# Kernel optimization log

Measured on AMD Instinct MI355X. Metric: run time of the kernel, lower is better.

## Reference

```python
import jax, jax.numpy as jnp
import numpy as np

B, T, I, H, O = 64, 256, 128, 512, 64
GRAD_CLIP = 5.0


def setup_inputs() -> dict:
    key = jax.random.key(0)
    ks = jax.random.split(key, 20)
    sH = 1.0 / np.sqrt(H)
    sI = 1.0 / np.sqrt(I)
    f32 = jnp.float32
    return {
        "x": jax.random.normal(ks[0], (B, T, I), f32),
        "y": jax.random.randint(ks[1], (B,), 0, O),
        "W1w": jax.random.normal(ks[2], (H, H), f32) * sH,
        "V1w": jax.random.normal(ks[3], (H, I), f32) * sI,
        "V1b": jnp.zeros((H,), f32),
        "W2w": jax.random.normal(ks[4], (H, H), f32) * sH,
        "W2b": jnp.zeros((H,), f32),
        "V2w": jax.random.normal(ks[5], (H, I), f32) * sI,
        "W3w": jax.random.normal(ks[6], (H, H), f32) * sH,
        "W3b": jnp.zeros((H,), f32),
        "V3w": jax.random.normal(ks[7], (H, I), f32) * sI,
        "Woutw": jax.random.normal(ks[8], (O, H), f32) * sH,
        "Woutb": jnp.zeros((O,), f32),
        "BW1": jax.random.normal(ks[9], (O, H), f32) * sH,
        "BV1": jax.random.normal(ks[10], (O, H), f32) * sH,
        "BW2": jax.random.normal(ks[11], (O, H), f32) * sH,
        "BV2": jax.random.normal(ks[12], (O, H), f32) * sH,
        "BW3": jax.random.normal(ks[13], (O, H), f32) * sH,
        "BV3": jax.random.normal(ks[14], (O, H), f32) * sH,
    }


def reference(x, y, W1w, V1w, V1b, W2w, W2b, V2w, W3w, W3b, V3w,
              Woutw, Woutb, BW1, BV1, BW2, BV2, BW3, BV3):
    Bsz, Tlen, _ = x.shape
    Hd = W1w.shape[0]
    Od = Woutw.shape[0]
    h0 = jnp.zeros((Bsz, Hd), x.dtype)
    xt = jnp.swapaxes(x, 0, 1)  # [T, B, I]

    def step(h, xti):
        z = jax.nn.sigmoid(h @ W2w.T + W2b + xti @ V2w.T)
        r = jax.nn.sigmoid(h @ W3w.T + W3b + xti @ V3w.T)
        ht = jnp.tanh(xti @ V1w.T + V1b + (h * r) @ W1w.T)
        hn = (1.0 - z) * ht + z * h
        return hn, (r, z, ht, hn)

    hT, (rs, zs, hs, hid) = jax.lax.scan(step, h0, xt)  # each [T, B, H]
    output = jax.nn.softmax(hT @ Woutw.T + Woutb, axis=-1)
    error = output - jax.nn.one_hot(y, Od, dtype=output.dtype)

    BW1e, BV1e = error @ BW1, error @ BV1
    BW2e, BV2e = error @ BW2, error @ BV2
    BW3e, BV3e = error @ BW3, error @ BV3

    hiddens = jnp.concatenate([h0[None], hid], axis=0)  # [T+1, B, H]
    # Faithfully replicate torch's hiddens[t-1] list indexing: at t=0 this is
    # hiddens[-1], i.e. the FINAL hidden state (Python negative indexing).
    idx = (np.arange(Tlen) - 1) % (Tlen + 1)
    hprev = hiddens[idx]  # [T, B, H]

    rr = rs * (1.0 - rs)
    sz = 1.0 - zs
    dh = 1.0 - hs ** 2

    # z-gate terms (index 1) -- original code uses r*(1-r) here, replicated.
    zg = (hprev - hs) * rr
    zgV = zg * BV2e[None]
    zgW = zg * BW2e[None]
    dV1 = jnp.einsum('tbh,tbi->hi', zgV, xt) / Bsz
    dW1 = jnp.einsum('tbh,tbH->hH', zgW, hprev) / Bsz
    db1 = zgV.sum(0).mean(0)

    # r-gate terms (index 2)
    AV = ((BV3e[None] * sz * dh) @ W1w.T) * hprev * rr
    AW = ((BW3e[None] * sz * dh) @ W1w.T) * hprev * rr
    dV2 = jnp.einsum('tbh,tbi->hi', AV, xt) / Bsz
    dW2 = jnp.einsum('tbh,tbH->hH', AW, hprev) / Bsz
    db2 = AV.sum(0).mean(0)

    # h-gate terms (index 0)
    HV = ((BV1e[None] * sz) @ W1w.T) * dh
    HW = ((BW1e[None] * sz) @ W1w.T) * dh
    dV0 = jnp.einsum('tbh,tbi->hi', HV, xt) / Bsz
    dW0 = jnp.einsum('tbh,tbH->hH', HW, rs * hprev) / Bsz
    db0 = HV.sum(0).mean(0)

    def nc(g):
        g = g / jnp.linalg.norm(g)
        return jnp.clip(g, -GRAD_CLIP, GRAD_CLIP)

    return (output, hT,
            nc(dW0), nc(dW1), nc(dW2),
            nc(dV0), nc(dV1), nc(dV2),
            nc(db0), nc(db1), nc(db2),
            error)
```

## Files before the change

### kernel.cpp

```cpp
#include <hip/hip_runtime.h>
#include <hip/hip_bf16.h>

#define DI __device__ __forceinline__

typedef __bf16 bf16x8 __attribute__((ext_vector_type(8)));
typedef __bf16 bf16x4 __attribute__((ext_vector_type(4)));
typedef __bf16 bf16x2 __attribute__((ext_vector_type(2)));
typedef float  f32x4  __attribute__((ext_vector_type(4)));
typedef unsigned long long ull;

static constexpr int Bc = 64, Tc = 256, Ic = 128, Hc = 512, Oc = 64;
static constexpr int TBc = Tc * Bc;
static constexpr size_t THW = (size_t)TBc * Hc;

static constexpr size_t O_OUT = 0;
static constexpr size_t O_HT  = 4096;
static constexpr size_t O_DW0 = 36864;
static constexpr size_t O_DV0 = 823296;
static constexpr size_t O_DB0 = 1019904;
static constexpr size_t O_ERR = 1021440;

static constexpr size_t W_SLOT = 1024;
static constexpr size_t W_DB   = 2048;
static constexpr size_t W_FLG  = 8192;
static constexpr size_t W_ERRW = 16384;
static constexpr size_t W_PROJ = 32768;
static constexpr size_t W_W1B  = 819200;
static constexpr size_t W_HX   = 1343488;
static constexpr size_t W_HRX  = 1474560;
static constexpr size_t W_XT   = 1605632;
static constexpr size_t W_HIST = 5799936;
static constexpr size_t W_PB   = 72908800;
static constexpr size_t W_NEED = W_PB + 100663296;


DI void st32_agent(float* p, float v) {
  __hip_atomic_store((unsigned int*)p, __float_as_uint(v),
                     __ATOMIC_RELAXED, __HIP_MEMORY_SCOPE_AGENT);
}
DI ull ld64_agent(const void* p) {
  return __hip_atomic_load((ull*)p, __ATOMIC_RELAXED, __HIP_MEMORY_SCOPE_AGENT);
}

DI void group_barrier(int* flags_g, int myslot, int bar, bool& dead) {
  __syncthreads();
  if (threadIdx.x == 0)
    __hip_atomic_store(&flags_g[myslot * 32], bar,
                       __ATOMIC_RELAXED, __HIP_MEMORY_SCOPE_AGENT);
  if (threadIdx.x < 64 && !dead) {
    const int l = threadIdx.x;
    int spins = 0;
    for (;;) {
      int v = bar;
      if (l < 16)
        v = __hip_atomic_load(&flags_g[l * 32],
                              __ATOMIC_RELAXED, __HIP_MEMORY_SCOPE_AGENT);
      if (__all(v >= bar)) break;
      __builtin_amdgcn_s_sleep(1);
      if (++spins > 4000000) { dead = true; break; }
    }
  }
  __syncthreads();
}

DI float hprev_at(const __bf16* __restrict__ h_h, int k, int col) {
  int t = k >> 6;
  if (t == 1) return 0.f;
  int row = (t == 0) ? (16320 + (k & 63)) : (k - 128);
  return (float)h_h[(size_t)row * 512 + col];
}


__global__ void kzero(float* __restrict__ p, int n) {
  int i = blockIdx.x * 256 + threadIdx.x;
  if (i < n) p[i] = 0.f;
}
__global__ void ksent(float* p, float v) { p[0] = v; }

__global__ __launch_bounds__(256)
void k1_xv(const float* __restrict__ x, const float* __restrict__ V1w,
           const float* __restrict__ V2w, const float* __restrict__ V3w,
           const float* __restrict__ V1b, const float* __restrict__ W2b,
           const float* __restrict__ W3b,
           float* __restrict__ xv1f, float* __restrict__ xv2f, float* __restrict__ xv3f)
{
  const int cb = blockIdx.x, t = blockIdx.y;
  const int g = cb >> 3, jblk = cb & 7;
  const float* Vg   = (g == 0) ? V1w : (g == 1) ? V2w : V3w;
  const float* bias = (g == 0) ? V1b : (g == 1) ? W2b : W3b;
  float* of = (g == 0) ? xv1f : (g == 1) ? xv2f : xv3f;
  __shared__ float As[64 * 69];
  __shared__ float Bs[64 * 69];
  const int tid = threadIdx.x;
  float acc[4][4] = {};
  const int m0 = (tid & 15) * 4, j0 = (tid >> 4) * 4;
  for (int kc = 0; kc < 2; ++kc) {
    __syncthreads();
    #pragma unroll
    for (int e = 0; e < 4; ++e) {
      int idx = tid + e * 256;
      int row = idx >> 4, c4 = (idx & 15) * 4;
      float4 v = *reinterpret_cast<const float4*>(&x[((size_t)row * 256 + t) * 128 + kc * 64 + c4]);
      As[row * 69 + c4 + 0] = v.x; As[row * 69 + c4 + 1] = v.y;
      As[row * 69 + c4 + 2] = v.z; As[row * 69 + c4 + 3] = v.w;
      float4 w = *reinterpret_cast<const float4*>(&Vg[(size_t)(jblk * 64 + row) * 128 + kc * 64 + c4]);
      Bs[row * 69 + c4 + 0] = w.x; Bs[row * 69 + c4 + 1] = w.y;
      Bs[row * 69 + c4 + 2] = w.z; Bs[row * 69 + c4 + 3] = w.w;
    }
    __syncthreads();
    for (int i = 0; i < 64; ++i) {
      float a[4], b[4];
      #pragma unroll
      for (int u = 0; u < 4; ++u) a[u] = As[(m0 + u) * 69 + i];
      #pragma unroll
      for (int u = 0; u < 4; ++u) b[u] = Bs[(j0 + u) * 69 + i];
      #pragma unroll
      for (int mi = 0; mi < 4; ++mi)
        #pragma unroll
        for (int ji = 0; ji < 4; ++ji) acc[mi][ji] += a[mi] * b[ji];
    }
  }
  #pragma unroll
  for (int ji = 0; ji < 4; ++ji) {
    int jg = jblk * 64 + j0 + ji;
    float bv = bias[jg];
    #pragma unroll
    for (int mi = 0; mi < 4; ++mi) {
      int b = m0 + mi;
      of[((size_t)t * 64 + b) * 512 + jg] = acc[mi][ji] + bv;
    }
  }
}

__global__ __launch_bounds__(256, 1)
void k2_recur(const float* __restrict__ W1w, const float* __restrict__ W2w,
              const float* __restrict__ W3w,
              const float* __restrict__ xv1, const float* __restrict__ xv2,
              const float* __restrict__ xv3,
              __bf16* __restrict__ r_h, __bf16* __restrict__ z_h,
              __bf16* __restrict__ ht_h, __bf16* __restrict__ h_h,
              float* __restrict__ hx, float* __restrict__ hrx,
              int* __restrict__ flags, float* __restrict__ dout,
              const float* __restrict__ x, __bf16* __restrict__ XT,
              __bf16* __restrict__ W1b)
{
  __shared__ __align__(16) char smem[37376];
  const int tid = threadIdx.x;
  const int bid = blockIdx.x;

  if (bid >= 64) {
    if (bid < 320) {
      const int t = bid - 64;
      __bf16* xs = (__bf16*)smem;
      #pragma unroll
      for (int e = 0; e < 8; ++e) {
        int idx = tid + e * 256;
        int b = idx >> 5, c4 = (idx & 31) * 4;
        float4 v = *reinterpret_cast<const float4*>(&x[((size_t)b * 256 + t) * 128 + c4]);
        xs[b * 132 + c4 + 0] = (__bf16)v.x; xs[b * 132 + c4 + 1] = (__bf16)v.y;
        xs[b * 132 + c4 + 2] = (__bf16)v.z; xs[b * 132 + c4 + 3] = (__bf16)v.w;
      }
      __syncthreads();
      #pragma unroll
      for (int e = 0; e < 8; ++e) {
        int idx = tid + e * 256;
        int i = idx >> 4, b4 = (idx & 15) * 4;
        __bf16* d = &XT[(size_t)i * TBc + t * 64 + b4];
        d[0] = xs[(b4 + 0) * 132 + i];
        d[1] = xs[(b4 + 1) * 132 + i];
        d[2] = xs[(b4 + 2) * 132 + i];
        d[3] = xs[(b4 + 3) * 132 + i];
      }
    } else if (bid < 352) {
      for (int i = (bid - 320) * 256 + tid; i < 262144; i += 32 * 256)
        W1b[i] = (__bf16)W1w[i];
    } else {
      float* p = dout + O_DW0;
      for (int i = (bid - 352) * 256 + tid; i < 983040; i += 64 * 256)
        p[i] = 0.f;
    }
    return;
  }

  const int g  = bid >> 4;
  const int cw = bid & 15;
  const int lane = tid & 63, wv = tid >> 6;
  const int kh = wv & 1;
  const int ct = wv >> 1;
  const int q  = lane >> 4;
  const int colc = cw * 32 + ct * 16 + (lane & 15);
  const bool owner = (kh == 0);

  __bf16* c0  = (__bf16*)smem;
  __bf16* c1  = (__bf16*)(smem + 16384);
  float*  pbuf = (float*)(smem + 32768);

  bf16x8 w1c[2][8], w2c[2][8], w3c[2][8];
  #pragma unroll
  for (int kk2 = 0; kk2 < 8; ++kk2) {
    const int kb = (kh * 8 + kk2) * 32 + q * 8;
    #pragma unroll
    for (int j = 0; j < 8; ++j) {
      float w = W1w[(size_t)colc * 512 + kb + j];
      __bf16 a = (__bf16)w;
      w1c[0][kk2][j] = a; w1c[1][kk2][j] = (__bf16)(w - (float)a);
      w = W2w[(size_t)colc * 512 + kb + j];
      a = (__bf16)w;
      w2c[0][kk2][j] = a; w2c[1][kk2][j] = (__bf16)(w - (float)a);
      w = W3w[(size_t)colc * 512 + kb + j];
      a = (__bf16)w;
      w3c[0][kk2][j] = a; w3c[1][kk2][j] = (__bf16)(w - (float)a);
    }
  }
  for (int i = tid; i < 8192; i += 256) {
    c0[i] = (__bf16)0.f; c1[i] = (__bf16)0.f;
  }
  __syncthreads();

  float hreg[4] = {0.f, 0.f, 0.f, 0.f};
  float* hx_g  = hx  + g * 8192;
  float* hrx_g = hrx + g * 8192;
  int* flags_g = flags + g * 16 * 32;
  const int fragbase = (colc >> 5) * 512 + (((colc >> 3) & 3) * 16 + q * 4) * 8 + (colc & 7);
  const int pb = (ct * 64 + lane) * 9;

  auto stage = [&](const float* __restrict__ srcf) {
    const ull* src = reinterpret_cast<const ull*>(srcf);
    ull u[16];
    #pragma unroll
    for (int j = 0; j < 16; ++j) u[j] = ld64_agent(src + j * 256 + tid);
    #pragma unroll
    for (int j = 0; j < 16; ++j) {
      float f0 = __uint_as_float((unsigned int)u[j]);
      float f1 = __uint_as_float((unsigned int)(u[j] >> 32));
      __bf16 a0 = (__bf16)f0; __bf16 b0 = (__bf16)(f0 - (float)a0);
      __bf16 a1 = (__bf16)f1; __bf16 b1 = (__bf16)(f1 - (float)a1);
      int o = (j * 256 + tid) * 2;
      bf16x2 v0; v0[0] = a0; v0[1] = a1;
      bf16x2 v1; v1[0] = b0; v1[1] = b1;
      *reinterpret_cast<bf16x2*>(&c0[o]) = v0;
      *reinterpret_cast<bf16x2*>(&c1[o]) = v1;
    }
  };

  bool dead = false;
  int bar = 0;
  #pragma unroll 1
  for (int t = 0; t < Tc; ++t) {
    const size_t rowb = ((size_t)t * 64 + g * 16 + q * 4) * 512 + colc;
    float xv1v[4], xv2v[4], xv3v[4];
    if (owner) {
      #pragma unroll
      for (int i = 0; i < 4; ++i) {
        size_t o = rowb + (size_t)i * 512;
        xv1v[i] = xv1[o]; xv2v[i] = xv2[o]; xv3v[i] = xv3[o];
      }
    }
    f32x4 a2 = {0.f,0.f,0.f,0.f}, a3 = {0.f,0.f,0.f,0.f};
    #pragma unroll
    for (int kk2 = 0; kk2 < 8; ++kk2) {
      const int idx = (kh * 8 + kk2) * 512 + lane * 8;
      bf16x8 h0 = *reinterpret_cast<const bf16x8*>(&c0[idx]);
      bf16x8 h1 = *reinterpret_cast<const bf16x8*>(&c1[idx]);
      a2 = __builtin_amdgcn_mfma_f32_16x16x32_bf16(h0, w2c[0][kk2], a2, 0, 0, 0);
      a2 = __builtin_amdgcn_mfma_f32_16x16x32_bf16(h1, w2c[0][kk2], a2, 0, 0, 0);
      a2 = __builtin_amdgcn_mfma_f32_16x16x32_bf16(h0, w2c[1][kk2], a2, 0, 0, 0);
      a3 = __builtin_amdgcn_mfma_f32_16x16x32_bf16(h0, w3c[0][kk2], a3, 0, 0, 0);
      a3 = __builtin_amdgcn_mfma_f32_16x16x32_bf16(h1, w3c[0][kk2], a3, 0, 0, 0);
      a3 = __builtin_amdgcn_mfma_f32_16x16x32_bf16(h0, w3c[1][kk2], a3, 0, 0, 0);
    }
    if (!owner) {
      #pragma unroll
      for (int i = 0; i < 4; ++i) { pbuf[pb + i] = a2[i]; pbuf[pb + 4 + i] = a3[i]; }
    }
    __syncthreads();
    float zz[4], rr4[4];
    if (owner) {
      #pragma unroll
      for (int i = 0; i < 4; ++i) {
        float s2 = a2[i] + pbuf[pb + i]     + xv2v[i];
        float s3 = a3[i] + pbuf[pb + 4 + i] + xv3v[i];
        zz[i]  = 1.f / (1.f + expf(-s2));
        rr4[i] = 1.f / (1.f + expf(-s3));
        st32_agent(&hrx_g[fragbase + i * 8], hreg[i] * rr4[i]);
      }
    }
    ++bar; group_barrier(flags_g, cw, bar, dead);
    if (owner) {
      #pragma unroll
      for (int i = 0; i < 4; ++i) {
        z_h[rowb + (size_t)i * 512] = (__bf16)zz[i];
        r_h[rowb + (size_t)i * 512] = (__bf16)rr4[i];
      }
    }
    stage(hrx_g);
    __syncthreads();
    f32x4 a1 = {0.f,0.f,0.f,0.f};
    #pragma unroll
    for (int kk2 = 0; kk2 < 8; ++kk2) {
      const int idx = (kh * 8 + kk2) * 512 + lane * 8;
      bf16x8 h0 = *reinterpret_cast<const bf16x8*>(&c0[idx]);
      bf16x8 h1 = *reinterpret_cast<const bf16x8*>(&c1[idx]);
      a1 = __builtin_amdgcn_mfma_f32_16x16x32_bf16(h0, w1c[0][kk2], a1, 0, 0, 0);
      a1 = __builtin_amdgcn_mfma_f32_16x16x32_bf16(h1, w1c[0][kk2], a1, 0, 0, 0);
      a1 = __builtin_amdgcn_mfma_f32_16x16x32_bf16(h0, w1c[1][kk2], a1, 0, 0, 0);
    }
    if (!owner) {
      #pragma unroll
      for (int i = 0; i < 4; ++i) pbuf[pb + i] = a1[i];
    }
    __syncthreads();
    float htv[4];
    if (owner) {
      #pragma unroll
      for (int i = 0; i < 4; ++i) {
        float pre = a1[i] + pbuf[pb + i] + xv1v[i];
        float ht = tanhf(pre);
        float hn = zz[i] * (hreg[i] - ht) + ht;
        htv[i] = ht;
        hreg[i] = hn;
        st32_agent(&hx_g[fragbase + i * 8], hn);
      }
    }
    ++bar; group_barrier(flags_g, cw, bar, dead);
    if (owner) {
      #pragma unroll
      for (int i = 0; i < 4; ++i) {
        ht_h[rowb + (size_t)i * 512] = (__bf16)htv[i];
        h_h[rowb + (size_t)i * 512]  = (__bf16)hreg[i];
      }
    }
    if (t + 1 < Tc) stage(hx_g);
    __syncthreads();
  }
  if (owner) {
    #pragma unroll
    for (int i = 0; i < 4; ++i) {
      int b = g * 16 + q * 4 + i;
      dout[O_HT + (size_t)b * 512 + colc] = hreg[i];
    }
  }
}

__global__ void k3a_soft(const float* __restrict__ Woutw, const float* __restrict__ Woutb,
                         const int* __restrict__ y, float* __restrict__ dout,
                         float* __restrict__ errw)
{
  const int b = blockIdx.x, o = threadIdx.x;
  const float* hrow = dout + O_HT + (size_t)b * 512;
  float sv = Woutb[o];
  for (int k = 0; k < 512; ++k) sv += hrow[k] * Woutw[(size_t)o * 512 + k];
  float mx = sv;
  for (int off = 32; off; off >>= 1) mx = fmaxf(mx, __shfl_xor(mx, off, 64));
  float e = expf(sv - mx);
  float sum = e;
  for (int off = 32; off; off >>= 1) sum += __shfl_xor(sum, off, 64);
  float outp = e / sum;
  float errv = outp - ((y[b] == o) ? 1.f : 0.f);
  dout[O_OUT + b * 64 + o] = outp;
  dout[O_ERR + b * 64 + o] = errv;
  errw[b * 64 + o] = errv;
}

__global__ __launch_bounds__(256)
void k3b_proj(const float* __restrict__ err,
              const float* b0, const float* b1, const float* b2,
              const float* b3, const float* b4, const float* b5,
              float* __restrict__ proj)
{
  const int p = blockIdx.y;
  const int hb = blockIdx.x * 64;
  const float* BX = (p==0)?b0:(p==1)?b1:(p==2)?b2:(p==3)?b3:(p==4)?b4:b5;
  __shared__ float es[64 * 64];
  __shared__ float bs[64 * 65];
  for (int i = threadIdx.x; i < 4096; i += 256) es[i] = err[i];
  for (int i = threadIdx.x; i < 4096; i += 256) {
    int o = i >> 6, hh = i & 63;
    bs[o * 65 + hh] = BX[(size_t)o * 512 + hb + hh];
  }
  __syncthreads();
  for (int e = 0; e < 16; ++e) {
    int idx = threadIdx.x + e * 256;
    int b = idx >> 6, hh = idx & 63;
    float s = 0.f;
    for (int o = 0; o < 64; ++o) s += es[b * 64 + o] * bs[o * 65 + hh];
    proj[(size_t)p * 32768 + b * 512 + hb + hh] = s;
  }
}

__global__ __launch_bounds__(256)
void e1t(const __bf16* __restrict__ r_h, const __bf16* __restrict__ h_h,
         __bf16* __restrict__ HpT, __bf16* __restrict__ RsHpT)
{
  const int t = blockIdx.y, hb = blockIdx.x * 64;
  const int tid = threadIdx.x;
  __shared__ __bf16 tr[64 * 68];
  float hpv[16], rv[16];
  #pragma unroll
  for (int e = 0; e < 16; ++e) {
    int idx = tid + e * 256;
    int b = idx >> 6, hl = idx & 63;
    hpv[e] = hprev_at(h_h, t * 64 + b, hb + hl);
    rv[e]  = (float)r_h[((size_t)t * 64 + b) * 512 + hb + hl];
  }
  for (int rnd = 0; rnd < 2; ++rnd) {
    __syncthreads();
    #pragma unroll
    for (int e = 0; e < 16; ++e) {
      int idx = tid + e * 256;
      int b = idx >> 6, hl = idx & 63;
      tr[b * 68 + hl] = (__bf16)(rnd == 0 ? hpv[e] : rv[e] * hpv[e]);
    }
    __syncthreads();
    __bf16* dst = (rnd == 0) ? HpT : RsHpT;
    #pragma unroll
    for (int e = 0; e < 16; ++e) {
      int idx = tid + e * 256;
      int hl2 = idx >> 6, b2 = idx & 63;
      dst[(size_t)(hb + hl2) * TBc + t * 64 + b2] = tr[b2 * 68 + hl2];
    }
  }
}

__global__ __launch_bounds__(256)
void k4_pgemm(const __bf16* __restrict__ z_h, const __bf16* __restrict__ ht_h,
              const __bf16* __restrict__ r_h, const __bf16* __restrict__ h_h,
              const float* __restrict__ proj, const __bf16* __restrict__ W1b,
              __bf16* __restrict__ P)
{
  const int p = blockIdx.z;
  const int krow0 = blockIdx.x * 128;
  const int n0 = blockIdx.y * 128;
  const int pidx = (p == 0) ? 5 : (p == 1) ? 4 : (p == 2) ? 1 : 0;
  const float* pr = proj + (size_t)pidx * 32768;
  const int tid = threadIdx.x, lane = tid & 63, wv = tid >> 6, q = lane >> 4;
  const int wm = (wv & 1) * 64, wn = (wv >> 1) * 64;
  __shared__ __align__(16) __bf16 Al[128 * 40];
  __shared__ __align__(16) __bf16 Bl[128 * 40];
  f32x4 acc[4][4] = {};
  for (int kt = 0; kt < 16; ++kt) {
    const int h0 = kt * 32;
    __syncthreads();
    #pragma unroll
    for (int e = 0; e < 4; ++e) {
      int idx = tid + e * 256;
      int row = idx >> 3, h4 = (idx & 7) * 4;
      int kg = krow0 + row;
      bf16x4 zz = *reinterpret_cast<const bf16x4*>(&z_h[(size_t)kg * 512 + h0 + h4]);
      bf16x4 tt = *reinterpret_cast<const bf16x4*>(&ht_h[(size_t)kg * 512 + h0 + h4]);
      float4 pv = *reinterpret_cast<const float4*>(&pr[(size_t)(kg & 63) * 512 + h0 + h4]);
      float pvv[4] = {pv.x, pv.y, pv.z, pv.w};
      bf16x4 gv;
      #pragma unroll
      for (int j = 0; j < 4; ++j) {
        float sz = 1.f - (float)zz[j];
        float v = pvv[j] * sz;
        if (p < 2) { float h = (float)tt[j]; v *= (1.f - h * h); }
        gv[j] = (__bf16)v;
      }
      *reinterpret_cast<bf16x4*>(&Al[row * 40 + h4]) = gv;
      bf16x4 wv4 = *reinterpret_cast<const bf16x4*>(&W1b[(size_t)(n0 + row) * 512 + h0 + h4]);
      *reinterpret_cast<bf16x4*>(&Bl[row * 40 + h4]) = wv4;
    }
    __syncthreads();
    bf16x8 af[4], bfv[4];
    #pragma unroll
    for (int mi = 0; mi < 4; ++mi)
      af[mi] = *reinterpret_cast<const bf16x8*>(&Al[(wm + mi * 16 + (lane & 15)) * 40 + q * 8]);
    #pragma unroll
    for (int ni = 0; ni < 4; ++ni)
      bfv[ni] = *reinterpret_cast<const bf16x8*>(&Bl[(wn + ni * 16 + (lane & 15)) * 40 + q * 8]);
    #pragma unroll
    for (int mi = 0; mi < 4; ++mi)
      #pragma unroll
      for (int ni = 0; ni < 4; ++ni)
        acc[mi][ni] = __builtin_amdgcn_mfma_f32_16x16x32_bf16(af[mi], bfv[ni], acc[mi][ni], 0, 0, 0);
  }
  __bf16* Pp = P + (size_t)p * THW;
  #pragma unroll
  for (int mi = 0; mi < 4; ++mi) {
    const int kg = krow0 + wm + mi * 16 + q * 4;
    const int tt = kg >> 6;
    #pragma unroll
    for (int ni = 0; ni < 4; ++ni) {
      const int n = n0 + wn + ni * 16 + (lane & 15);
      union { __bf16 b[4]; uint2 u; } pk;
      #pragma unroll
      for (int i = 0; i < 4; ++i) {
        float mul;
        if (p < 2) {
          float r = (float)r_h[(size_t)(kg + i) * 512 + n];
          float hp = 0.f;
          if (tt != 1) {
            int kr = (tt == 0) ? (16320 + (kg & 63) + i) : (kg + i - 128);
            hp = (float)h_h[(size_t)kr * 512 + n];
          }
          mul = hp * r * (1.f - r);
        } else {
          float h = (float)ht_h[(size_t)(kg + i) * 512 + n];
          mul = 1.f - h * h;
        }
        pk.b[i] = (__bf16)(acc[mi][ni][i] * mul);
      }
      *reinterpret_cast<uint2*>(&Pp[(size_t)n * TBc + kg]) = pk.u;
    }
  }
}

__global__ __launch_bounds__(256)
void k5_all(const __bf16* __restrict__ P, const __bf16* __restrict__ RsHpT,
            const __bf16* __restrict__ HpT, const __bf16* __restrict__ XT,
            const __bf16* __restrict__ r_h, const __bf16* __restrict__ ht_h,
            const __bf16* __restrict__ h_h, const float* __restrict__ proj,
            float* __restrict__ dout, float scale)
{
  const __bf16* Ap; int amode; const __bf16* Bp; const float* projA;
  float* out; int N; int m0i, n0i, zi;
  int b = blockIdx.x;
  if (b < 768) {
    int job = b >> 8, wb = b & 255;
    m0i = wb & 3; n0i = (wb >> 2) & 3; zi = wb >> 4;
    N = 512;
    out = dout + O_DW0 + (size_t)job * 262144;
    if (job == 0)      { Ap = P + 3 * THW; amode = 0; Bp = RsHpT; projA = proj; }
    else if (job == 1) { Ap = nullptr;     amode = 1; Bp = HpT;   projA = proj + 2 * 32768; }
    else               { Ap = P + 1 * THW; amode = 0; Bp = HpT;   projA = proj; }
  } else {
    int b2 = b - 768; int job = b2 >> 6, wb = b2 & 63;
    m0i = wb & 3; n0i = 0; zi = wb >> 2;
    N = 128;
    out = dout + O_DV0 + (size_t)job * 65536;
    if (job == 0)      { Ap = P + 2 * THW; amode = 0; Bp = XT; projA = proj; }
    else if (job == 1) { Ap = nullptr;     amode = 1; Bp = XT; projA = proj + 3 * 32768; }
    else               { Ap = P + 0 * THW; amode = 0; Bp = XT; projA = proj; }
  }
  const int m0 = m0i * 128;
  const int n0 = n0i * 128;
  const int klen = 1024;
  const int tid = threadIdx.x, lane = tid & 63, wv = tid >> 6, q = lane >> 4;
  const int wm = (wv & 1) * 64, wn = (wv >> 1) * 64;
  __shared__ __align__(16) __bf16 Al[128 * 72];
  __shared__ __align__(16) __bf16 Bl[128 * 72];
  f32x4 acc[4][4] = {};
  const int iters = klen >> 6;
  for (int kt = 0; kt < iters; ++kt) {
    const int kk0 = zi * klen + kt * 64;
    __syncthreads();
    #pragma unroll
    for (int e = 0; e < 8; ++e) {
      int idx = tid + e * 256;
      int row = idx >> 4, c4 = (idx & 15) * 4;
      bf16x4 bv = *reinterpret_cast<const bf16x4*>(&Bp[(size_t)(n0 + row) * TBc + kk0 + c4]);
      *reinterpret_cast<bf16x4*>(&Bl[row * 72 + c4]) = bv;
    }
    if (amode == 0) {
      #pragma unroll
      for (int e = 0; e < 8; ++e) {
        int idx = tid + e * 256;
        int row = idx >> 4, c4 = (idx & 15) * 4;
        bf16x4 av = *reinterpret_cast<const bf16x4*>(&Ap[(size_t)(m0 + row) * TBc + kk0 + c4]);
        *reinterpret_cast<bf16x4*>(&Al[row * 72 + c4]) = av;
      }
    } else {
      #pragma unroll
      for (int e = 0; e < 8; ++e) {
        int idx = tid + e * 256;
        int kk = idx >> 5;
        int m4 = (idx & 31) * 4;
        int kg = kk0 + kk;
        int tt = kg >> 6;
        bf16x4 hs = *reinterpret_cast<const bf16x4*>(&ht_h[(size_t)kg * 512 + m0 + m4]);
        bf16x4 rv = *reinterpret_cast<const bf16x4*>(&r_h[(size_t)kg * 512 + m0 + m4]);
        float4 pv = *reinterpret_cast<const float4*>(&projA[(size_t)(kg & 63) * 512 + m0 + m4]);
        float pvv[4] = {pv.x, pv.y, pv.z, pv.w};
        float hpf[4] = {0.f, 0.f, 0.f, 0.f};
        if (tt != 1) {
          int kr = (tt == 0) ? (16320 + (kg & 63)) : (kg - 128);
          bf16x4 hp = *reinterpret_cast<const bf16x4*>(&h_h[(size_t)kr * 512 + m0 + m4]);
          #pragma unroll
          for (int j = 0; j < 4; ++j) hpf[j] = (float)hp[j];
        }
        #pragma unroll
        for (int j = 0; j < 4; ++j) {
          float r = (float)rv[j];
          float zg = (hpf[j] - (float)hs[j]) * r * (1.f - r) * pvv[j];
          Al[(m4 + j) * 72 + kk] = (__bf16)zg;
        }
      }
    }
    __syncthreads();
    #pragma unroll
    for (int ks = 0; ks < 2; ++ks) {
      bf16x8 af[4], bfv[4];
      #pragma unroll
      for (int mi = 0; mi < 4; ++mi)
        af[mi] = *reinterpret_cast<const bf16x8*>(&Al[(wm + mi * 16 + (lane & 15)) * 72 + ks * 32 + q * 8]);
      #pragma unroll
      for (int ni = 0; ni < 4; ++ni)
        bfv[ni] = *reinterpret_cast<const bf16x8*>(&Bl[(wn + ni * 16 + (lane & 15)) * 72 + ks * 32 + q * 8]);
      #pragma unroll
      for (int mi = 0; mi < 4; ++mi)
        #pragma unroll
        for (int ni = 0; ni < 4; ++ni)
          acc[mi][ni] = __builtin_amdgcn_mfma_f32_16x16x32_bf16(af[mi], bfv[ni], acc[mi][ni], 0, 0, 0);
    }
  }
  #pragma unroll
  for (int mi = 0; mi < 4; ++mi) {
    const int m = m0 + wm + mi * 16 + q * 4;
    #pragma unroll
    for (int ni = 0; ni < 4; ++ni) {
      const int n = n0 + wn + ni * 16 + (lane & 15);
      #pragma unroll
      for (int i = 0; i < 4; ++i)
        atomicAdd(&out[(size_t)(m + i) * N + n], acc[mi][ni][i] * scale);
    }
  }
}

__global__ void k_dbP(const __bf16* __restrict__ P, float* __restrict__ db)
{
  const size_t plane = (blockIdx.y == 0) ? 2 : 0;
  const int dbo = (blockIdx.y == 0) ? 0 : 1024;
  const __bf16* row = P + plane * THW + (size_t)blockIdx.x * TBc;
  float sv = 0.f;
  for (int i = threadIdx.x; i < TBc; i += 256) sv += (float)row[i];
  for (int off = 32; off; off >>= 1) sv += __shfl_xor(sv, off, 64);
  __shared__ float red[4];
  if ((threadIdx.x & 63) == 0) red[threadIdx.x >> 6] = sv;
  __syncthreads();
  if (threadIdx.x == 0)
    atomicAdd(&db[dbo + blockIdx.x], (red[0] + red[1] + red[2] + red[3]) * (1.f / 64.f));
}

__global__ void k_dbzg(const __bf16* __restrict__ r_h, const __bf16* __restrict__ ht_h,
                       const __bf16* __restrict__ h_h, const float* __restrict__ proj,
                       float* __restrict__ db)
{
  const int hb = blockIdx.x * 64;
  const int col = hb + (threadIdx.x & 63);
  const int part = threadIdx.x >> 6;
  const int kb = blockIdx.y * 1024;
  float sum = 0.f;
  for (int k = kb + part; k < kb + 1024; k += 4) {
    float hs = (float)ht_h[(size_t)k * 512 + col];
    float r  = (float)r_h[(size_t)k * 512 + col];
    float hp = hprev_at(h_h, k, col);
    float pv = proj[3 * 32768 + (size_t)(k & 63) * 512 + col];
    sum += (hp - hs) * r * (1.f - r) * pv;
  }
  __shared__ float sred[4][64];
  sred[part][threadIdx.x & 63] = sum;
  __syncthreads();
  if (threadIdx.x < 64)
    atomicAdd(&db[512 + hb + threadIdx.x],
              (sred[0][threadIdx.x] + sred[1][threadIdx.x] +
               sred[2][threadIdx.x] + sred[3][threadIdx.x]) * (1.f / 64.f));
}

__global__ void k6a_sumsq(const float* __restrict__ dout, const float* __restrict__ db,
                          float* __restrict__ slots)
{
  const int yy = blockIdx.y;
  const float* src; int count;
  if (yy < 3)      { src = dout + O_DW0 + (size_t)yy * 262144; count = 262144; }
  else if (yy < 6) { src = dout + O_DV0 + (size_t)(yy - 3) * 65536; count = 65536; }
  else             { src = db + (size_t)(yy - 6) * 512; count = 512; }
  int start = blockIdx.x * 4096;
  if (start >= count) return;
  int end = min(start + 4096, count);
  float sp = 0.f;
  for (int i = start + threadIdx.x; i < end; i += 256) { float v = src[i]; sp += v * v; }
  for (int off = 32; off; off >>= 1) sp += __shfl_xor(sp, off, 64);
  __shared__ float red[4];
  if ((threadIdx.x & 63) == 0) red[threadIdx.x >> 6] = sp;
  __syncthreads();
  if (threadIdx.x == 0) atomicAdd(&slots[yy], red[0] + red[1] + red[2] + red[3]);
}

__global__ void k6b_write(const float* __restrict__ db,
                          const float* __restrict__ slots, float* __restrict__ dout)
{
  const int yy = blockIdx.y;
  const float* src; int count; size_t oo;
  if (yy < 3)      { oo = O_DW0 + (size_t)yy * 262144; src = dout + oo; count = 262144; }
  else if (yy < 6) { oo = O_DV0 + (size_t)(yy - 3) * 65536; src = dout + oo; count = 65536; }
  else             { oo = O_DB0 + (size_t)(yy - 6) * 512; src = db + (size_t)(yy - 6) * 512; count = 512; }
  int start = blockIdx.x * 4096;
  if (start >= count) return;
  int end = min(start + 4096, count);
  float inv = 1.f / sqrtf(slots[yy]);
  for (int i = start + threadIdx.x; i < end; i += 256) {
    float v = src[i] * inv;
    dout[oo + i] = fminf(fmaxf(v, -5.f), 5.f);
  }
}

extern "C" void kernel_launch(void* const* d_in, const int* in_sizes, int n_in,
                              void* d_out, int out_size, void* d_ws, size_t ws_size,
                              hipStream_t stream)
{
  const float* x     = (const float*)d_in[0];
  const int*   y     = (const int*)d_in[1];
  const float* W1w   = (const float*)d_in[2];
  const float* V1w   = (const float*)d_in[3];
  const float* V1b   = (const float*)d_in[4];
  const float* W2w   = (const float*)d_in[5];
  const float* W2b   = (const float*)d_in[6];
  const float* V2w   = (const float*)d_in[7];
  const float* W3w   = (const float*)d_in[8];
  const float* W3b   = (const float*)d_in[9];
  const float* V3w   = (const float*)d_in[10];
  const float* Woutw = (const float*)d_in[11];
  const float* Woutb = (const float*)d_in[12];
  const float* BW1   = (const float*)d_in[13];
  const float* BV1   = (const float*)d_in[14];
  const float* BW2   = (const float*)d_in[15];
  const float* BV2   = (const float*)d_in[16];
  const float* BW3   = (const float*)d_in[17];
  const float* BV3   = (const float*)d_in[18];
  float* dout = (float*)d_out;
  char* ws = (char*)d_ws;

  if (ws_size < W_NEED) { ksent<<<1, 1, 0, stream>>>(dout, (float)ws_size); return; }

  float*  slots = (float*)(ws + W_SLOT);
  float*  dbr   = (float*)(ws + W_DB);
  int*    flg   = (int*)(ws + W_FLG);
  float*  errw  = (float*)(ws + W_ERRW);
  float*  proj  = (float*)(ws + W_PROJ);
  __bf16* W1b   = (__bf16*)(ws + W_W1B);
  float*  hx    = (float*)(ws + W_HX);
  float*  hrx   = (float*)(ws + W_HRX);
  __bf16* XT    = (__bf16*)(ws + W_XT);
  __bf16* r_h   = (__bf16*)(ws + W_HIST);
  __bf16* z_h   = (__bf16*)(ws + W_HIST + 16777216);
  __bf16* ht_h  = (__bf16*)(ws + W_HIST + 33554432);
  __bf16* h_h   = (__bf16*)(ws + W_HIST + 50331648);
  char*   PB    = ws + W_PB;

  float* xv1 = (float*)PB;
  float* xv2 = (float*)(PB + 33554432);
  float* xv3 = (float*)(PB + 67108864);
  __bf16* P     = (__bf16*)PB;
  __bf16* HpT   = (__bf16*)(PB + 67108864);
  __bf16* RsHpT = (__bf16*)(PB + 83886080);

  kzero<<<16, 256, 0, stream>>>((float*)ws, 4096);
  k1_xv<<<dim3(24, 256), 256, 0, stream>>>(x, V1w, V2w, V3w, V1b, W2b, W3b, xv1, xv2, xv3);
  k2_recur<<<416, 256, 0, stream>>>(W1w, W2w, W3w, xv1, xv2, xv3,
                                    r_h, z_h, ht_h, h_h, hx, hrx, flg, dout,
                                    x, XT, W1b);
  k3a_soft<<<64, 64, 0, stream>>>(Woutw, Woutb, y, dout, errw);
  k3b_proj<<<dim3(8, 6), 256, 0, stream>>>(errw, BW1, BV1, BW2, BV2, BW3, BV3, proj);
  e1t<<<dim3(8, 256), 256, 0, stream>>>(r_h, h_h, HpT, RsHpT);
  k_dbzg<<<dim3(8, 16), 256, 0, stream>>>(r_h, ht_h, h_h, proj, dbr);

  k4_pgemm<<<dim3(128, 4, 4), 256, 0, stream>>>(z_h, ht_h, r_h, h_h, proj, W1b, P);
  const float sc = 1.f / 64.f;
  k5_all<<<960, 256, 0, stream>>>(P, RsHpT, HpT, XT, r_h, ht_h, h_h, proj, dout, sc);
  k_dbP<<<dim3(512, 2), 256, 0, stream>>>(P, dbr);
  k6a_sumsq<<<dim3(64, 9), 256, 0, stream>>>(dout, dbr, slots);
  k6b_write<<<dim3(64, 9), 256, 0, stream>>>(dbr, slots, dout);
}
```

Measured before the change: 2.372 ms.

## Merge backward kernels, share W1 tiles in pgemm, and use split-bf16 MFMA for input projection

Four changes at once. The input projection now runs on MFMA with a three-term bf16 hi/lo split that approximates fp32, and each block loops over all eight column blocks. The transpose kernel is folded into the softmax launch, and the two bias-reduction kernels are folded into the weight-gradient GEMM launch, cutting launch count. The P GEMM computes two projection planes per block so W1 tiles are loaded once for both. This trades extra registers and LDS for fewer launches and less reloading, with a small precision change in the input projection.

```diff
diff --git a/kernel.cpp b/kernel.cpp
--- a/kernel.cpp
+++ b/kernel.cpp
@@ -84,51 +84,67 @@
            const float* __restrict__ W3b,
            float* __restrict__ xv1f, float* __restrict__ xv2f, float* __restrict__ xv3f)
 {
-  const int cb = blockIdx.x, t = blockIdx.y;
-  const int g = cb >> 3, jblk = cb & 7;
+  const int t = blockIdx.x, g = blockIdx.y;
   const float* Vg   = (g == 0) ? V1w : (g == 1) ? V2w : V3w;
   const float* bias = (g == 0) ? V1b : (g == 1) ? W2b : W3b;
   float* of = (g == 0) ? xv1f : (g == 1) ? xv2f : xv3f;
-  __shared__ float As[64 * 69];
-  __shared__ float Bs[64 * 69];
-  const int tid = threadIdx.x;
-  float acc[4][4] = {};
-  const int m0 = (tid & 15) * 4, j0 = (tid >> 4) * 4;
-  for (int kc = 0; kc < 2; ++kc) {
-    __syncthreads();
-    #pragma unroll
-    for (int e = 0; e < 4; ++e) {
-      int idx = tid + e * 256;
-      int row = idx >> 4, c4 = (idx & 15) * 4;
-      float4 v = *reinterpret_cast<const float4*>(&x[((size_t)row * 256 + t) * 128 + kc * 64 + c4]);
-      As[row * 69 + c4 + 0] = v.x; As[row * 69 + c4 + 1] = v.y;
-      As[row * 69 + c4 + 2] = v.z; As[row * 69 + c4 + 3] = v.w;
-      float4 w = *reinterpret_cast<const float4*>(&Vg[(size_t)(jblk * 64 + row) * 128 + kc * 64 + c4]);
-      Bs[row * 69 + c4 + 0] = w.x; Bs[row * 69 + c4 + 1] = w.y;
-      Bs[row * 69 + c4 + 2] = w.z; Bs[row * 69 + c4 + 3] = w.w;
-    }
-    __syncthreads();
-    for (int i = 0; i < 64; ++i) {
-      float a[4], b[4];
-      #pragma unroll
-      for (int u = 0; u < 4; ++u) a[u] = As[(m0 + u) * 69 + i];
-      #pragma unroll
-      for (int u = 0; u < 4; ++u) b[u] = Bs[(j0 + u) * 69 + i];
-      #pragma unroll
-      for (int mi = 0; mi < 4; ++mi)
+  __shared__ __align__(16) __bf16 xs0[64 * 36];
+  __shared__ __align__(16) __bf16 xs1[64 * 36];
+  __shared__ __align__(16) __bf16 vs0[64 * 36];
+  __shared__ __align__(16) __bf16 vs1[64 * 36];
+  const int tid = threadIdx.x, lane = tid & 63, wv = tid >> 6;
+  const int q = lane >> 4, l15 = lane & 15;
+  for (int cb = 0; cb < 8; ++cb) {
+    f32x4 acc[4];
+    #pragma unroll
+    for (int mt = 0; mt < 4; ++mt) acc[mt] = (f32x4){0.f, 0.f, 0.f, 0.f};
+    for (int kc = 0; kc < 4; ++kc) {
+      __syncthreads();
+      #pragma unroll
+      for (int e = 0; e < 2; ++e) {
+        int idx = tid + e * 256;
+        int row = idx >> 3, k4 = (idx & 7) * 4;
+        float4 v = *reinterpret_cast<const float4*>(&x[((size_t)row * 256 + t) * 128 + kc * 32 + k4]);
+        float fv[4] = {v.x, v.y, v.z, v.w};
+        bf16x4 a4, b4;
         #pragma unroll
-        for (int ji = 0; ji < 4; ++ji) acc[mi][ji] += a[mi] * b[ji];
-    }
-  }
-  #pragma unroll
-  for (int ji = 0; ji < 4; ++ji) {
-    int jg = jblk * 64 + j0 + ji;
-    float bv = bias[jg];
-    #pragma unroll
-    for (int mi = 0; mi < 4; ++mi) {
-      int b = m0 + mi;
-      of[((size_t)t * 64 + b) * 512 + jg] = acc[mi][ji] + bv;
-    }
+        for (int j = 0; j < 4; ++j) {
+          __bf16 a = (__bf16)fv[j];
+          a4[j] = a; b4[j] = (__bf16)(fv[j] - (float)a);
+        }
+        *reinterpret_cast<bf16x4*>(&xs0[row * 36 + k4]) = a4;
+        *reinterpret_cast<bf16x4*>(&xs1[row * 36 + k4]) = b4;
+        float4 w = *reinterpret_cast<const float4*>(&Vg[(size_t)(cb * 64 + row) * 128 + kc * 32 + k4]);
+        float fw[4] = {w.x, w.y, w.z, w.w};
+        #pragma unroll
+        for (int j = 0; j < 4; ++j) {
+          __bf16 a = (__bf16)fw[j];
+          a4[j] = a; b4[j] = (__bf16)(fw[j] - (float)a);
+        }
+        *reinterpret_cast<bf16x4*>(&vs0[row * 36 + k4]) = a4;
+        *reinterpret_cast<bf16x4*>(&vs1[row * 36 + k4]) = b4;
+      }
+      __syncthreads();
+      bf16x8 b0 = *reinterpret_cast<const bf16x8*>(&vs0[(wv * 16 + l15) * 36 + q * 8]);
+      bf16x8 b1 = *reinterpret_cast<const bf16x8*>(&vs1[(wv * 16 + l15) * 36 + q * 8]);
+      #pragma unroll
+      for (int mt = 0; mt < 4; ++mt) {
+        bf16x8 a0 = *reinterpret_cast<const bf16x8*>(&xs0[(mt * 16 + l15) * 36 + q * 8]);
+        bf16x8 a1 = *reinterpret_cast<const bf16x8*>(&xs1[(mt * 16 + l15) * 36 + q * 8]);
+        acc[mt] = __builtin_amdgcn_mfma_f32_16x16x32_bf16(a0, b0, acc[mt], 0, 0, 0);
+        acc[mt] = __builtin_amdgcn_mfma_f32_16x16x32_bf16(a1, b0, acc[mt], 0, 0, 0);
+        acc[mt] = __builtin_amdgcn_mfma_f32_16x16x32_bf16(a0, b1, acc[mt], 0, 0, 0);
+      }
+    }
+    const int col = cb * 64 + wv * 16 + l15;
+    const float bv = bias[col];
+    #pragma unroll
+    for (int mt = 0; mt < 4; ++mt)
+      #pragma unroll
+      for (int i = 0; i < 4; ++i) {
+        int row = mt * 16 + q * 4 + i;
+        of[((size_t)t * 64 + row) * 512 + col] = acc[mt][i] + bv;
+      }
   }
 }
 
@@ -342,24 +358,60 @@
   }
 }
 
-__global__ void k3a_soft(const float* __restrict__ Woutw, const float* __restrict__ Woutb,
-                         const int* __restrict__ y, float* __restrict__ dout,
-                         float* __restrict__ errw)
-{
-  const int b = blockIdx.x, o = threadIdx.x;
-  const float* hrow = dout + O_HT + (size_t)b * 512;
-  float sv = Woutb[o];
-  for (int k = 0; k < 512; ++k) sv += hrow[k] * Woutw[(size_t)o * 512 + k];
-  float mx = sv;
-  for (int off = 32; off; off >>= 1) mx = fmaxf(mx, __shfl_xor(mx, off, 64));
-  float e = expf(sv - mx);
-  float sum = e;
-  for (int off = 32; off; off >>= 1) sum += __shfl_xor(sum, off, 64);
-  float outp = e / sum;
-  float errv = outp - ((y[b] == o) ? 1.f : 0.f);
-  dout[O_OUT + b * 64 + o] = outp;
-  dout[O_ERR + b * 64 + o] = errv;
-  errw[b * 64 + o] = errv;
+__global__ __launch_bounds__(256)
+void k3m(const __bf16* __restrict__ r_h, const __bf16* __restrict__ h_h,
+         const float* __restrict__ Woutw, const float* __restrict__ Woutb,
+         const int* __restrict__ y, float* __restrict__ dout,
+         float* __restrict__ errw, __bf16* __restrict__ HpT,
+         __bf16* __restrict__ RsHpT)
+{
+  __shared__ __align__(16) char smem[8704];
+  const int bid = blockIdx.x, tid = threadIdx.x;
+  if (bid < 2048) {
+    const int t = bid >> 3, hb = (bid & 7) * 64;
+    __bf16* tr = (__bf16*)smem;
+    float hpv[16], rv[16];
+    #pragma unroll
+    for (int e = 0; e < 16; ++e) {
+      int idx = tid + e * 256;
+      int b = idx >> 6, hl = idx & 63;
+      hpv[e] = hprev_at(h_h, t * 64 + b, hb + hl);
+      rv[e]  = (float)r_h[((size_t)t * 64 + b) * 512 + hb + hl];
+    }
+    for (int rnd = 0; rnd < 2; ++rnd) {
+      __syncthreads();
+      #pragma unroll
+      for (int e = 0; e < 16; ++e) {
+        int idx = tid + e * 256;
+        int b = idx >> 6, hl = idx & 63;
+        tr[b * 68 + hl] = (__bf16)(rnd == 0 ? hpv[e] : rv[e] * hpv[e]);
+      }
+      __syncthreads();
+      __bf16* dst = (rnd == 0) ? HpT : RsHpT;
+      #pragma unroll
+      for (int e = 0; e < 16; ++e) {
+        int idx = tid + e * 256;
+        int hl2 = idx >> 6, b2 = idx & 63;
+        dst[(size_t)(hb + hl2) * TBc + t * 64 + b2] = tr[b2 * 68 + hl2];
+      }
+    }
+  } else {
+    const int b = (bid - 2048) * 4 + (tid >> 6);
+    const int o = tid & 63;
+    const float* hrow = dout + O_HT + (size_t)b * 512;
+    float sv = Woutb[o];
+    for (int k = 0; k < 512; ++k) sv += hrow[k] * Woutw[(size_t)o * 512 + k];
+    float mx = sv;
+    for (int off = 32; off; off >>= 1) mx = fmaxf(mx, __shfl_xor(mx, off, 64));
+    float e = expf(sv - mx);
+    float sum = e;
+    for (int off = 32; off; off >>= 1) sum += __shfl_xor(sum, off, 64);
+    float outp = e / sum;
+    float errv = outp - ((y[b] == o) ? 1.f : 0.f);
+    dout[O_OUT + b * 64 + o] = outp;
+    dout[O_ERR + b * 64 + o] = errv;
+    errw[b * 64 + o] = errv;
+  }
 }
 
 __global__ __launch_bounds__(256)
@@ -389,55 +441,22 @@
 }
 
 __global__ __launch_bounds__(256)
-void e1t(const __bf16* __restrict__ r_h, const __bf16* __restrict__ h_h,
-         __bf16* __restrict__ HpT, __bf16* __restrict__ RsHpT)
-{
-  const int t = blockIdx.y, hb = blockIdx.x * 64;
-  const int tid = threadIdx.x;
-  __shared__ __bf16 tr[64 * 68];
-  float hpv[16], rv[16];
-  #pragma unroll
-  for (int e = 0; e < 16; ++e) {
-    int idx = tid + e * 256;
-    int b = idx >> 6, hl = idx & 63;
-    hpv[e] = hprev_at(h_h, t * 64 + b, hb + hl);
-    rv[e]  = (float)r_h[((size_t)t * 64 + b) * 512 + hb + hl];
-  }
-  for (int rnd = 0; rnd < 2; ++rnd) {
-    __syncthreads();
-    #pragma unroll
-    for (int e = 0; e < 16; ++e) {
-      int idx = tid + e * 256;
-      int b = idx >> 6, hl = idx & 63;
-      tr[b * 68 + hl] = (__bf16)(rnd == 0 ? hpv[e] : rv[e] * hpv[e]);
-    }
-    __syncthreads();
-    __bf16* dst = (rnd == 0) ? HpT : RsHpT;
-    #pragma unroll
-    for (int e = 0; e < 16; ++e) {
-      int idx = tid + e * 256;
-      int hl2 = idx >> 6, b2 = idx & 63;
-      dst[(size_t)(hb + hl2) * TBc + t * 64 + b2] = tr[b2 * 68 + hl2];
-    }
-  }
-}
-
-__global__ __launch_bounds__(256)
 void k4_pgemm(const __bf16* __restrict__ z_h, const __bf16* __restrict__ ht_h,
               const __bf16* __restrict__ r_h, const __bf16* __restrict__ h_h,
               const float* __restrict__ proj, const __bf16* __restrict__ W1b,
               __bf16* __restrict__ P)
 {
-  const int p = blockIdx.z;
+  const int pp = blockIdx.z;
   const int krow0 = blockIdx.x * 128;
   const int n0 = blockIdx.y * 128;
-  const int pidx = (p == 0) ? 5 : (p == 1) ? 4 : (p == 2) ? 1 : 0;
-  const float* pr = proj + (size_t)pidx * 32768;
+  const float* prA = proj + (size_t)(pp == 0 ? 5 : 1) * 32768;
+  const float* prB = proj + (size_t)(pp == 0 ? 4 : 0) * 32768;
   const int tid = threadIdx.x, lane = tid & 63, wv = tid >> 6, q = lane >> 4;
   const int wm = (wv & 1) * 64, wn = (wv >> 1) * 64;
-  __shared__ __align__(16) __bf16 Al[128 * 40];
+  __shared__ __align__(16) __bf16 Al0[128 * 40];
+  __shared__ __align__(16) __bf16 Al1[128 * 40];
   __shared__ __align__(16) __bf16 Bl[128 * 40];
-  f32x4 acc[4][4] = {};
+  f32x4 acc0[4][4] = {}, acc1[4][4] = {};
   for (int kt = 0; kt < 16; ++kt) {
     const int h0 = kt * 32;
     __syncthreads();
@@ -447,36 +466,54 @@
       int row = idx >> 3, h4 = (idx & 7) * 4;
       int kg = krow0 + row;
       bf16x4 zz = *reinterpret_cast<const bf16x4*>(&z_h[(size_t)kg * 512 + h0 + h4]);
-      bf16x4 tt = *reinterpret_cast<const bf16x4*>(&ht_h[(size_t)kg * 512 + h0 + h4]);
-      float4 pv = *reinterpret_cast<const float4*>(&pr[(size_t)(kg & 63) * 512 + h0 + h4]);
-      float pvv[4] = {pv.x, pv.y, pv.z, pv.w};
-      bf16x4 gv;
-      #pragma unroll
-      for (int j = 0; j < 4; ++j) {
-        float sz = 1.f - (float)zz[j];
-        float v = pvv[j] * sz;
-        if (p < 2) { float h = (float)tt[j]; v *= (1.f - h * h); }
-        gv[j] = (__bf16)v;
-      }
-      *reinterpret_cast<bf16x4*>(&Al[row * 40 + h4]) = gv;
+      float4 pva = *reinterpret_cast<const float4*>(&prA[(size_t)(kg & 63) * 512 + h0 + h4]);
+      float4 pvb = *reinterpret_cast<const float4*>(&prB[(size_t)(kg & 63) * 512 + h0 + h4]);
+      float pA[4] = {pva.x, pva.y, pva.z, pva.w};
+      float pB[4] = {pvb.x, pvb.y, pvb.z, pvb.w};
+      bf16x4 gv0, gv1;
+      if (pp == 0) {
+        bf16x4 tt = *reinterpret_cast<const bf16x4*>(&ht_h[(size_t)kg * 512 + h0 + h4]);
+        #pragma unroll
+        for (int j = 0; j < 4; ++j) {
+          float sz = 1.f - (float)zz[j];
+          float h = (float)tt[j];
+          float f = sz * (1.f - h * h);
+          gv0[j] = (__bf16)(pA[j] * f);
+          gv1[j] = (__bf16)(pB[j] * f);
+        }
+      } else {
+        #pragma unroll
+        for (int j = 0; j < 4; ++j) {
+          float sz = 1.f - (float)zz[j];
+          gv0[j] = (__bf16)(pA[j] * sz);
+          gv1[j] = (__bf16)(pB[j] * sz);
+        }
+      }
+      *reinterpret_cast<bf16x4*>(&Al0[row * 40 + h4]) = gv0;
+      *reinterpret_cast<bf16x4*>(&Al1[row * 40 + h4]) = gv1;
       bf16x4 wv4 = *reinterpret_cast<const bf16x4*>(&W1b[(size_t)(n0 + row) * 512 + h0 + h4]);
       *reinterpret_cast<bf16x4*>(&Bl[row * 40 + h4]) = wv4;
     }
     __syncthreads();
-    bf16x8 af[4], bfv[4];
-    #pragma unroll
-    for (int mi = 0; mi < 4; ++mi)
-      af[mi] = *reinterpret_cast<const bf16x8*>(&Al[(wm + mi * 16 + (lane & 15)) * 40 + q * 8]);
+    bf16x8 af0[4], af1[4], bfv[4];
+    #pragma unroll
+    for (int mi = 0; mi < 4; ++mi) {
+      af0[mi] = *reinterpret_cast<const bf16x8*>(&Al0[(wm + mi * 16 + (lane & 15)) * 40 + q * 8]);
+      af1[mi] = *reinterpret_cast<const bf16x8*>(&Al1[(wm + mi * 16 + (lane & 15)) * 40 + q * 8]);
+    }
     #pragma unroll
     for (int ni = 0; ni < 4; ++ni)
       bfv[ni] = *reinterpret_cast<const bf16x8*>(&Bl[(wn + ni * 16 + (lane & 15)) * 40 + q * 8]);
     #pragma unroll
     for (int mi = 0; mi < 4; ++mi)
       #pragma unroll
-      for (int ni = 0; ni < 4; ++ni)
-        acc[mi][ni] = __builtin_amdgcn_mfma_f32_16x16x32_bf16(af[mi], bfv[ni], acc[mi][ni], 0, 0, 0);
-  }
-  __bf16* Pp = P + (size_t)p * THW;
+      for (int ni = 0; ni < 4; ++ni) {
+        acc0[mi][ni] = __builtin_amdgcn_mfma_f32_16x16x32_bf16(af0[mi], bfv[ni], acc0[mi][ni], 0, 0, 0);
+        acc1[mi][ni] = __builtin_amdgcn_mfma_f32_16x16x32_bf16(af1[mi], bfv[ni], acc1[mi][ni], 0, 0, 0);
+      }
+  }
+  __bf16* Pp0 = P + (size_t)(2 * pp) * THW;
+  __bf16* Pp1 = P + (size_t)(2 * pp + 1) * THW;
   #pragma unroll
   for (int mi = 0; mi < 4; ++mi) {
     const int kg = krow0 + wm + mi * 16 + q * 4;
@@ -484,11 +521,11 @@
     #pragma unroll
     for (int ni = 0; ni < 4; ++ni) {
       const int n = n0 + wn + ni * 16 + (lane & 15);
-      union { __bf16 b[4]; uint2 u; } pk;
+      union { __bf16 b[4]; uint2 u; } pk0, pk1;
       #pragma unroll
       for (int i = 0; i < 4; ++i) {
         float mul;
-        if (p < 2) {
+        if (pp == 0) {
           float r = (float)r_h[(size_t)(kg + i) * 512 + n];
           float hp = 0.f;
           if (tt != 1) {
@@ -500,25 +537,66 @@
           float h = (float)ht_h[(size_t)(kg + i) * 512 + n];
           mul = 1.f - h * h;
         }
-        pk.b[i] = (__bf16)(acc[mi][ni][i] * mul);
-      }
-      *reinterpret_cast<uint2*>(&Pp[(size_t)n * TBc + kg]) = pk.u;
+        pk0.b[i] = (__bf16)(acc0[mi][ni][i] * mul);
+        pk1.b[i] = (__bf16)(acc1[mi][ni][i] * mul);
+      }
+      *reinterpret_cast<uint2*>(&Pp0[(size_t)n * TBc + kg]) = pk0.u;
+      *reinterpret_cast<uint2*>(&Pp1[(size_t)n * TBc + kg]) = pk1.u;
     }
   }
 }
 
 __global__ __launch_bounds__(256)
-void k5_all(const __bf16* __restrict__ P, const __bf16* __restrict__ RsHpT,
-            const __bf16* __restrict__ HpT, const __bf16* __restrict__ XT,
-            const __bf16* __restrict__ r_h, const __bf16* __restrict__ ht_h,
-            const __bf16* __restrict__ h_h, const float* __restrict__ proj,
-            float* __restrict__ dout, float scale)
-{
+void k5m(const __bf16* __restrict__ P, const __bf16* __restrict__ RsHpT,
+         const __bf16* __restrict__ HpT, const __bf16* __restrict__ XT,
+         const __bf16* __restrict__ r_h, const __bf16* __restrict__ ht_h,
+         const __bf16* __restrict__ h_h, const float* __restrict__ proj,
+         float* __restrict__ dout, float* __restrict__ db, float scale)
+{
+  __shared__ __align__(16) char smem[36864];
+  const int bid = blockIdx.x, tid = threadIdx.x;
+  if (bid >= 1984) {
+    const int b2 = bid - 1984;
+    const int hb = (b2 & 7) * 64;
+    const int col = hb + (tid & 63);
+    const int part = tid >> 6;
+    const int kb = (b2 >> 3) * 1024;
+    float sum = 0.f;
+    for (int k = kb + part; k < kb + 1024; k += 4) {
+      float hs = (float)ht_h[(size_t)k * 512 + col];
+      float r  = (float)r_h[(size_t)k * 512 + col];
+      float hp = hprev_at(h_h, k, col);
+      float pv = proj[3 * 32768 + (size_t)(k & 63) * 512 + col];
+      sum += (hp - hs) * r * (1.f - r) * pv;
+    }
+    float (*sred)[64] = (float(*)[64])smem;
+    sred[part][tid & 63] = sum;
+    __syncthreads();
+    if (tid < 64)
+      atomicAdd(&db[512 + hb + tid],
+                (sred[0][tid] + sred[1][tid] + sred[2][tid] + sred[3][tid]) * (1.f / 64.f));
+    return;
+  }
+  if (bid >= 960) {
+    const int idx = bid - 960;
+    const size_t plane = ((idx >> 9) == 0) ? 2 : 0;
+    const int dbo = ((idx >> 9) == 0) ? 0 : 1024;
+    const int xrow = idx & 511;
+    const __bf16* row = P + plane * THW + (size_t)xrow * TBc;
+    float sv = 0.f;
+    for (int i = tid; i < TBc; i += 256) sv += (float)row[i];
+    for (int off = 32; off; off >>= 1) sv += __shfl_xor(sv, off, 64);
+    float* red = (float*)smem;
+    if ((tid & 63) == 0) red[tid >> 6] = sv;
+    __syncthreads();
+    if (tid == 0)
+      atomicAdd(&db[dbo + xrow], (red[0] + red[1] + red[2] + red[3]) * (1.f / 64.f));
+    return;
+  }
   const __bf16* Ap; int amode; const __bf16* Bp; const float* projA;
   float* out; int N; int m0i, n0i, zi;
-  int b = blockIdx.x;
-  if (b < 768) {
-    int job = b >> 8, wb = b & 255;
+  if (bid < 768) {
+    int job = bid >> 8, wb = bid & 255;
     m0i = wb & 3; n0i = (wb >> 2) & 3; zi = wb >> 4;
     N = 512;
     out = dout + O_DW0 + (size_t)job * 262144;
@@ -526,7 +604,7 @@
     else if (job == 1) { Ap = nullptr;     amode = 1; Bp = HpT;   projA = proj + 2 * 32768; }
     else               { Ap = P + 1 * THW; amode = 0; Bp = HpT;   projA = proj; }
   } else {
-    int b2 = b - 768; int job = b2 >> 6, wb = b2 & 63;
+    int b2 = bid - 768; int job = b2 >> 6, wb = b2 & 63;
     m0i = wb & 3; n0i = 0; zi = wb >> 2;
     N = 128;
     out = dout + O_DV0 + (size_t)job * 65536;
@@ -537,10 +615,10 @@
   const int m0 = m0i * 128;
   const int n0 = n0i * 128;
   const int klen = 1024;
-  const int tid = threadIdx.x, lane = tid & 63, wv = tid >> 6, q = lane >> 4;
+  const int lane = tid & 63, wv = tid >> 6, q = lane >> 4;
   const int wm = (wv & 1) * 64, wn = (wv >> 1) * 64;
-  __shared__ __align__(16) __bf16 Al[128 * 72];
-  __shared__ __align__(16) __bf16 Bl[128 * 72];
+  __bf16* Al = (__bf16*)smem;
+  __bf16* Bl = (__bf16*)(smem + 18432);
   f32x4 acc[4][4] = {};
   const int iters = klen >> 6;
   for (int kt = 0; kt < iters; ++kt) {
@@ -618,46 +696,6 @@
   }
 }
 
-__global__ void k_dbP(const __bf16* __restrict__ P, float* __restrict__ db)
-{
-  const size_t plane = (blockIdx.y == 0) ? 2 : 0;
-  const int dbo = (blockIdx.y == 0) ? 0 : 1024;
-  const __bf16* row = P + plane * THW + (size_t)blockIdx.x * TBc;
-  float sv = 0.f;
-  for (int i = threadIdx.x; i < TBc; i += 256) sv += (float)row[i];
-  for (int off = 32; off; off >>= 1) sv += __shfl_xor(sv, off, 64);
-  __shared__ float red[4];
-  if ((threadIdx.x & 63) == 0) red[threadIdx.x >> 6] = sv;
-  __syncthreads();
-  if (threadIdx.x == 0)
-    atomicAdd(&db[dbo + blockIdx.x], (red[0] + red[1] + red[2] + red[3]) * (1.f / 64.f));
-}
-
-__global__ void k_dbzg(const __bf16* __restrict__ r_h, const __bf16* __restrict__ ht_h,
-                       const __bf16* __restrict__ h_h, const float* __restrict__ proj,
-                       float* __restrict__ db)
-{
-  const int hb = blockIdx.x * 64;
-  const int col = hb + (threadIdx.x & 63);
-  const int part = threadIdx.x >> 6;
-  const int kb = blockIdx.y * 1024;
-  float sum = 0.f;
-  for (int k = kb + part; k < kb + 1024; k += 4) {
-    float hs = (float)ht_h[(size_t)k * 512 + col];
-    float r  = (float)r_h[(size_t)k * 512 + col];
-    float hp = hprev_at(h_h, k, col);
-    float pv = proj[3 * 32768 + (size_t)(k & 63) * 512 + col];
-    sum += (hp - hs) * r * (1.f - r) * pv;
-  }
-  __shared__ float sred[4][64];
-  sred[part][threadIdx.x & 63] = sum;
-  __syncthreads();
-  if (threadIdx.x < 64)
-    atomicAdd(&db[512 + hb + threadIdx.x],
-              (sred[0][threadIdx.x] + sred[1][threadIdx.x] +
-               sred[2][threadIdx.x] + sred[3][threadIdx.x]) * (1.f / 64.f));
-}
-
 __global__ void k6a_sumsq(const float* __restrict__ dout, const float* __restrict__ db,
                           float* __restrict__ slots)
 {
@@ -747,19 +785,15 @@
   __bf16* RsHpT = (__bf16*)(PB + 83886080);
 
   kzero<<<16, 256, 0, stream>>>((float*)ws, 4096);
-  k1_xv<<<dim3(24, 256), 256, 0, stream>>>(x, V1w, V2w, V3w, V1b, W2b, W3b, xv1, xv2, xv3);
+  k1_xv<<<dim3(256, 3), 256, 0, stream>>>(x, V1w, V2w, V3w, V1b, W2b, W3b, xv1, xv2, xv3);
   k2_recur<<<416, 256, 0, stream>>>(W1w, W2w, W3w, xv1, xv2, xv3,
                                     r_h, z_h, ht_h, h_h, hx, hrx, flg, dout,
                                     x, XT, W1b);
-  k3a_soft<<<64, 64, 0, stream>>>(Woutw, Woutb, y, dout, errw);
+  k3m<<<2064, 256, 0, stream>>>(r_h, h_h, Woutw, Woutb, y, dout, errw, HpT, RsHpT);
   k3b_proj<<<dim3(8, 6), 256, 0, stream>>>(errw, BW1, BV1, BW2, BV2, BW3, BV3, proj);
-  e1t<<<dim3(8, 256), 256, 0, stream>>>(r_h, h_h, HpT, RsHpT);
-  k_dbzg<<<dim3(8, 16), 256, 0, stream>>>(r_h, ht_h, h_h, proj, dbr);
-
-  k4_pgemm<<<dim3(128, 4, 4), 256, 0, stream>>>(z_h, ht_h, r_h, h_h, proj, W1b, P);
+  k4_pgemm<<<dim3(128, 4, 2), 256, 0, stream>>>(z_h, ht_h, r_h, h_h, proj, W1b, P);
   const float sc = 1.f / 64.f;
-  k5_all<<<960, 256, 0, stream>>>(P, RsHpT, HpT, XT, r_h, ht_h, h_h, proj, dout, sc);
-  k_dbP<<<dim3(512, 2), 256, 0, stream>>>(P, dbr);
+  k5m<<<2112, 256, 0, stream>>>(P, RsHpT, HpT, XT, r_h, ht_h, h_h, proj, dout, dbr, sc);
   k6a_sumsq<<<dim3(64, 9), 256, 0, stream>>>(dout, dbr, slots);
   k6b_write<<<dim3(64, 9), 256, 0, stream>>>(dbr, slots, dout);
 }
```

New measurement: 2.288 ms (median of 2 runs). 3.5% less time.
